# Kernel optimization log

Measured on AMD Instinct MI355X. Metric: run time of the kernel, lower is better.

## Reference

```python
import jax, jax.numpy as jnp
import numpy as np

D_MODEL = 1024
N_HEADS = 16
HEAD_DIM = D_MODEL // N_HEADS  # 64
BATCH = 2
SEQ = 2048
THETA = 10000.0


def _rope_tables(theta, d_k, max_seq_len):
    # matches RoPE.__init__: d = theta**(2*arange(d_k//2)/d_k); t = s / d
    inv = theta ** (2.0 * jnp.arange(0, d_k // 2, dtype=jnp.float32) / d_k)  # [d_k//2]
    s = jnp.arange(max_seq_len, dtype=jnp.float32)[:, None]  # [S,1]
    t = s / inv[None, :]  # [S, d_k//2]
    return jnp.sin(t), jnp.cos(t)


def setup_inputs() -> dict:
    key = jax.random.key(0)
    ks = jax.random.split(key, 5)
    std = np.sqrt(2.0 / (D_MODEL + D_MODEL))
    x = jax.random.normal(ks[0], (BATCH, SEQ, D_MODEL), dtype=jnp.float32)
    Wq = jax.random.normal(ks[1], (D_MODEL, D_MODEL), dtype=jnp.float32) * std
    Wk = jax.random.normal(ks[2], (D_MODEL, D_MODEL), dtype=jnp.float32) * std
    Wv = jax.random.normal(ks[3], (D_MODEL, D_MODEL), dtype=jnp.float32) * std
    Wo = jax.random.normal(ks[4], (D_MODEL, D_MODEL), dtype=jnp.float32) * std
    token_positions = jnp.arange(SEQ, dtype=jnp.int64)
    rope_sin, rope_cos = _rope_tables(THETA, HEAD_DIM, SEQ)
    return {"x": x, "token_positions": token_positions, "Wq": Wq, "Wk": Wk,
            "Wv": Wv, "Wo": Wo, "rope_sin": rope_sin, "rope_cos": rope_cos}


def _apply_rope(x, sin, cos):
    # x: [B, H, S, d_k]; sin/cos: [S, d_k//2] (gathered by token_positions)
    x1 = x[..., ::2]
    x2 = x[..., 1::2]
    x_even = x1 * cos - x2 * sin
    x_odd = x1 * sin + x2 * cos
    # interleave back: stack on last dim then flatten
    return jnp.stack([x_even, x_odd], axis=-1).reshape(x.shape)


def reference(x, token_positions, Wq, Wk, Wv, Wo, rope_sin, rope_cos):
    b, s, _ = x.shape
    h, d = N_HEADS, HEAD_DIM

    def proj(W):
        y = jnp.einsum('oi,bsi->bso', W, x)
        return y.reshape(b, s, h, d).transpose(0, 2, 1, 3)  # [b, h, s, d]

    q = proj(Wq)
    k = proj(Wk)
    v = proj(Wv)

    sin = rope_sin[token_positions]  # [s, d//2]
    cos = rope_cos[token_positions]
    q = _apply_rope(q, sin, cos)
    k = _apply_rope(k, sin, cos)

    # causal scaled-dot-product attention (FlashAttention.apply(..., True))
    scale = 1.0 / jnp.sqrt(jnp.asarray(d, dtype=x.dtype))
    scores = jnp.einsum('bhqd,bhkd->bhqk', q, k) * scale
    causal = jnp.tril(jnp.ones((s, s), dtype=bool))
    scores = jnp.where(causal, scores, jnp.finfo(x.dtype).min)
    attn = jax.nn.softmax(scores, axis=-1)
    out = jnp.einsum('bhqk,bhkd->bhqd', attn, v)  # [b, h, s, d]
    out = out.transpose(0, 2, 1, 3).reshape(b, s, h * d)
    return jnp.einsum('oi,bsi->bso', Wo, out)
```

## Files before the change

kernel.cpp:

```cpp
#include <hip/hip_runtime.h>
#include <hip/hip_bf16.h>
#include <math.h>

#define BATCH   2
#define S_LEN   2048
#define DM      1024
#define NH      16
#define HD      64
#define MROWS   4096

typedef __hip_bfloat16 bf16;
typedef __attribute__((ext_vector_type(8))) short short8;
typedef __attribute__((ext_vector_type(4))) float float4v;

#define QSCALE 0.18033688011112043f

#define WC_VM0   0x0F70
#define WC_VM4   0x0F74
#define WC_VM6   0x0F76
#define WC_VM8   0x0F78
#define WC_VM12  0x0F7C
#define WC_LGKM0 0xC07F

__device__ __forceinline__ short f2s(float x) {
    union { bf16 h; short s; } u; u.h = __float2bfloat16(x); return u.s;
}
__device__ __forceinline__ short8 load8(const void* p) {
    return *reinterpret_cast<const short8*>(p);
}
__device__ __forceinline__ void cvt8(const float* g, bf16* d) {
    float4v a = *reinterpret_cast<const float4v*>(g);
    float4v b = *reinterpret_cast<const float4v*>(g + 4);
    short8 r;
    r[0] = f2s(a[0]); r[1] = f2s(a[1]); r[2] = f2s(a[2]); r[3] = f2s(a[3]);
    r[4] = f2s(b[0]); r[5] = f2s(b[1]); r[6] = f2s(b[2]); r[7] = f2s(b[3]);
    *reinterpret_cast<short8*>(d) = r;
}
__device__ __forceinline__ void gll16(const void* g, void* l) {
    __builtin_amdgcn_global_load_lds(
        (const __attribute__((address_space(1))) unsigned int*)g,
        (__attribute__((address_space(3))) unsigned int*)l,
        16, 0, 0);
}
__device__ __forceinline__ unsigned pack2(float a, float b) {
    union { float f; unsigned u; } ua, ub;
    ua.f = a; ub.f = b;
    return ((ua.u + 0x8000u) >> 16) | ((ub.u + 0x8000u) & 0xFFFF0000u);
}

__global__ __launch_bounds__(256) void cvt_kernel(const float* __restrict__ x,
                                                  const float* __restrict__ wq,
                                                  const float* __restrict__ wk,
                                                  const float* __restrict__ wv,
                                                  const float* __restrict__ wo,
                                                  bf16* __restrict__ xb,
                                                  bf16* __restrict__ wqb,
                                                  bf16* __restrict__ wkb,
                                                  bf16* __restrict__ wvb,
                                                  bf16* __restrict__ wob) {
    const size_t i = ((size_t)blockIdx.x * 256 + threadIdx.x) * 8;
    const size_t NX = (size_t)MROWS * DM;
    const size_t NW = (size_t)DM * DM;
    if (i < NX)                { cvt8(x  + i,               xb  + i); }
    else if (i < NX + NW)      { cvt8(wq + (i - NX),        wqb + (i - NX)); }
    else if (i < NX + 2 * NW)  { cvt8(wk + (i - NX - NW),   wkb + (i - NX - NW)); }
    else if (i < NX + 3 * NW)  { cvt8(wv + (i - NX - 2*NW), wvb + (i - NX - 2*NW)); }
    else                       { cvt8(wo + (i - NX - 3*NW), wob + (i - NX - 3*NW)); }
}

__global__ __launch_bounds__(256) void qkv_gemm(const bf16* __restrict__ A,
                                                const bf16* __restrict__ Wqb,
                                                const bf16* __restrict__ Wkb,
                                                const bf16* __restrict__ Wvb,
                                                bf16* __restrict__ Qb, bf16* __restrict__ Kb,
                                                bf16* __restrict__ Vtb,
                                                const float* __restrict__ rsin,
                                                const float* __restrict__ rcos) {
    __shared__ short As[3][64 * 64];
    __shared__ short Bs[3][64 * 64];

    const int j    = threadIdx.x;
    const int w    = j >> 6;
    const int lane = j & 63;
    const int quad = lane >> 4;
    const int lid  = lane & 15;
    const int wm   = w & 1, wn = w >> 1;

    const int mb  = blockIdx.x * 128;
    const int sel = blockIdx.y >> 3;
    const int nb  = (blockIdx.y & 7) * 128;
    const bf16* W = (sel == 0) ? Wqb : (sel == 1) ? Wkb : Wvb;

    int sOff[2];
#pragma unroll
    for (int i = 0; i < 2; ++i) {
        const int u  = (i * 4 + w) * 64 + lane;
        const int rp = u >> 3;
        const int ch = (u & 7) ^ (rp & 7);
        const int gr = ((ch >> 2) << 6) + rp;
        const int gc = ch & 3;
        sOff[i] = gr * DM + gc * 8;
    }
    const bf16* baseA = A + (size_t)mb * DM;
    const bf16* baseB = W + (size_t)nb * DM;

#pragma unroll
    for (int t = 0; t < 2; ++t) {
#pragma unroll
        for (int i = 0; i < 2; ++i) gll16(baseA + t * 32 + sOff[i], &As[t][(i * 4 + w) * 512]);
#pragma unroll
        for (int i = 0; i < 2; ++i) gll16(baseB + t * 32 + sOff[i], &Bs[t][(i * 4 + w) * 512]);
    }

    int aRd[4], bRd[4];
#pragma unroll
    for (int t = 0; t < 4; ++t) {
        aRd[t] = (t * 16 + lid) * 64 + (((wm * 4 + quad) ^ (lid & 7)) * 8);
        bRd[t] = (t * 16 + lid) * 64 + (((wn * 4 + quad) ^ (lid & 7)) * 8);
    }

    float4v acc[4][4] = {};
    int buf = 0;
    for (int it = 0; it < 32; ++it) {
        __builtin_amdgcn_s_barrier();
        if (it < 30) {
            const int k0 = (it + 2) * 32;
            const int b = (buf + 2 >= 3) ? buf - 1 : buf + 2;
#pragma unroll
            for (int i = 0; i < 2; ++i) gll16(baseA + k0 + sOff[i], &As[b][(i * 4 + w) * 512]);
#pragma unroll
            for (int i = 0; i < 2; ++i) gll16(baseB + k0 + sOff[i], &Bs[b][(i * 4 + w) * 512]);
            __builtin_amdgcn_s_waitcnt(WC_VM8);
        } else if (it == 30) {
            __builtin_amdgcn_s_waitcnt(WC_VM4);
        } else {
            __builtin_amdgcn_s_waitcnt(WC_VM0);
        }
        __builtin_amdgcn_s_barrier();

        const short* as = As[buf];
        const short* bs = Bs[buf];
        short8 af[4], bfr[4];
#pragma unroll
        for (int mt = 0; mt < 4; ++mt) af[mt] = load8(&as[aRd[mt]]);
#pragma unroll
        for (int nt = 0; nt < 4; ++nt) bfr[nt] = load8(&bs[bRd[nt]]);
#pragma unroll
        for (int mt = 0; mt < 4; ++mt)
#pragma unroll
            for (int nt = 0; nt < 4; ++nt)
                acc[mt][nt] = __builtin_amdgcn_mfma_f32_16x16x32_bf16(af[mt], bfr[nt], acc[mt][nt], 0, 0, 0);
        buf = (buf == 2) ? 0 : buf + 1;
    }

#pragma unroll
    for (int mt = 0; mt < 4; ++mt) {
#pragma unroll
        for (int nt = 0; nt < 4; ++nt) {
            const int n = nb + wn * 64 + nt * 16 + lid;
            const int h = n >> 6, d = n & 63;
#pragma unroll
            for (int r = 0; r < 4; ++r) {
                const int m = mb + wm * 64 + mt * 16 + quad * 4 + r;
                const int s = m & (S_LEN - 1), bi = m >> 11;
                float val = acc[mt][nt][r];
                if (sel == 0) val *= QSCALE;
                float par = __shfl_xor(val, 1, 64);
                if (sel == 2) {
                    Vtb[(((size_t)bi * NH + h) * HD + d) * S_LEN + s] = __float2bfloat16(val);
                } else {
                    const float sn = rsin[s * 32 + (d >> 1)];
                    const float cs = rcos[s * 32 + (d >> 1)];
                    const float v = ((d & 1) == 0) ? val * cs - par * sn
                                                   : par * sn + val * cs;
                    bf16* dst = (sel == 0) ? Qb : Kb;
                    dst[(((size_t)bi * NH + h) * S_LEN + s) * HD + d] = __float2bfloat16(v);
                }
            }
        }
    }
}

__global__ __launch_bounds__(256) void out_gemm(const bf16* __restrict__ A,
                                                const bf16* __restrict__ W,
                                                float* __restrict__ out) {
    __shared__ short As[3][128 * 64];
    __shared__ short Bs[3][64 * 64];

    const int j    = threadIdx.x;
    const int w    = j >> 6;
    const int lane = j & 63;
    const int quad = lane >> 4;
    const int lid  = lane & 15;

    const int mb = blockIdx.x * 128;
    const int nb = blockIdx.y * 64;

    int aOff[4], bOff[2];
#pragma unroll
    for (int i = 0; i < 4; ++i) {
        const int u = i * 256 + j;
        const int r = u >> 3;
        const int c = (u & 7) ^ (r & 7);
        aOff[i] = r * DM + c * 8;
    }
#pragma unroll
    for (int i = 0; i < 2; ++i) {
        const int u = i * 256 + j;
        const int r = u >> 3;
        const int c = (u & 7) ^ (r & 7);
        bOff[i] = r * DM + c * 8;
    }
    const bf16* baseA = A + (size_t)mb * DM;
    const bf16* baseB = W + (size_t)nb * DM;

#pragma unroll
    for (int t = 0; t < 2; ++t) {
#pragma unroll
        for (int i = 0; i < 4; ++i) gll16(baseA + t * 64 + aOff[i], &As[t][(i * 256 + w * 64) * 8]);
#pragma unroll
        for (int i = 0; i < 2; ++i) gll16(baseB + t * 64 + bOff[i], &Bs[t][(i * 256 + w * 64) * 8]);
    }

    int aRd[2], bRd[4];
#pragma unroll
    for (int mt = 0; mt < 2; ++mt) {
        const int ra = w * 32 + mt * 16 + lid;
        aRd[mt] = ra * 64 + ((quad ^ (lid & 7)) * 8);
    }
#pragma unroll
    for (int nt = 0; nt < 4; ++nt) {
        const int rb = nt * 16 + lid;
        bRd[nt] = rb * 64 + ((quad ^ (lid & 7)) * 8);
    }

    float4v acc[2][4] = {};
    int buf = 0;
    for (int it = 0; it < 16; ++it) {
        __builtin_amdgcn_s_barrier();
        if (it < 14) {
            const int k0 = (it + 2) * 64;
            const int b = (buf + 2 >= 3) ? buf - 1 : buf + 2;
#pragma unroll
            for (int i = 0; i < 4; ++i) gll16(baseA + k0 + aOff[i], &As[b][(i * 256 + w * 64) * 8]);
#pragma unroll
            for (int i = 0; i < 2; ++i) gll16(baseB + k0 + bOff[i], &Bs[b][(i * 256 + w * 64) * 8]);
            __builtin_amdgcn_s_waitcnt(WC_VM12);
        } else if (it == 14) {
            __builtin_amdgcn_s_waitcnt(WC_VM6);
        } else {
            __builtin_amdgcn_s_waitcnt(WC_VM0);
        }
        __builtin_amdgcn_s_barrier();

        const short* as = As[buf];
        const short* bs = Bs[buf];
        short8 af[2][2], bfr[4][2];
#pragma unroll
        for (int mt = 0; mt < 2; ++mt)
#pragma unroll
            for (int ks = 0; ks < 2; ++ks) af[mt][ks] = load8(&as[aRd[mt] ^ (ks * 32)]);
#pragma unroll
        for (int nt = 0; nt < 4; ++nt)
#pragma unroll
            for (int ks = 0; ks < 2; ++ks) bfr[nt][ks] = load8(&bs[bRd[nt] ^ (ks * 32)]);
#pragma unroll
        for (int mt = 0; mt < 2; ++mt)
#pragma unroll
            for (int nt = 0; nt < 4; ++nt)
#pragma unroll
                for (int ks = 0; ks < 2; ++ks)
                    acc[mt][nt] = __builtin_amdgcn_mfma_f32_16x16x32_bf16(af[mt][ks], bfr[nt][ks], acc[mt][nt], 0, 0, 0);
        buf = (buf == 2) ? 0 : buf + 1;
    }

#pragma unroll
    for (int mt = 0; mt < 2; ++mt)
#pragma unroll
        for (int nt = 0; nt < 4; ++nt) {
            const int n = nb + nt * 16 + lid;
#pragma unroll
            for (int r = 0; r < 4; ++r) {
                const int m = mb + w * 32 + mt * 16 + quad * 4 + r;
                out[(size_t)m * DM + n] = acc[mt][nt][r];
            }
        }
}

__global__ __launch_bounds__(256) void flash6(const bf16* __restrict__ Q,
                                              const bf16* __restrict__ K,
                                              const bf16* __restrict__ Vt,
                                              bf16* __restrict__ att) {
    __shared__ short Ks[128 * 64];
    __shared__ short Vs[64 * 128];
    __shared__ short Pb[128 * 128];

    const int j    = threadIdx.x;
    const int w    = j >> 6;
    const int lane = j & 63;
    const int quad = lane >> 4;
    const int lid  = lane & 15;
    const int bh   = blockIdx.x;
    const int by   = blockIdx.y;
    const int qt   = (by < 8) ? (15 - by) : (by - 8);
    const int bi   = bh >> 4, h = bh & 15;
    const int qb   = qt * 128;

    const size_t bh_off = (size_t)bh * S_LEN * HD;
    const bf16* Qp = Q + bh_off;
    const bf16* Kp = K + bh_off;
    const bf16* Vp = Vt + bh_off;

    short8 aQ[2][2];
#pragma unroll
    for (int mm = 0; mm < 2; ++mm)
#pragma unroll
        for (int kf = 0; kf < 2; ++kf)
            aQ[mm][kf] = load8(Qp + (size_t)(qb + w * 32 + mm * 16 + lid) * HD + kf * 32 + quad * 8);

    int kOff[4], vOff[4];
#pragma unroll
    for (int i = 0; i < 4; ++i) {
        const int idx = (i * 4 + w) * 64 + lane;
        const int kr = idx >> 3, kc = (idx & 7) ^ (kr & 7);
        kOff[i] = kr * HD + kc * 8;
        const int vr = idx >> 4, vc = (idx & 15) ^ (vr & 15);
        vOff[i] = vr * S_LEN + vc * 8;
    }

    float4v accO[2][4] = {};
    float4v accS[2] = {};
    short8 ones;
#pragma unroll
    for (int t = 0; t < 8; ++t) ones[t] = (short)0x3F80;

    short8 kReg[4], vReg[4];
#pragma unroll
    for (int i = 0; i < 4; ++i) kReg[i] = load8(Kp + kOff[i]);
#pragma unroll
    for (int i = 0; i < 4; ++i) vReg[i] = load8(Vp + vOff[i]);

    const int nkt = qt + 1;
    for (int kti = 0; kti < nkt; ++kti) {
        __builtin_amdgcn_s_barrier();
#pragma unroll
        for (int i = 0; i < 4; ++i)
            *reinterpret_cast<short8*>(&Ks[(i * 4 + w) * 512 + lane * 8]) = kReg[i];
#pragma unroll
        for (int i = 0; i < 4; ++i)
            *reinterpret_cast<short8*>(&Vs[(i * 4 + w) * 512 + lane * 8]) = vReg[i];
        if (kti + 1 < nkt) {
            const int ktn = (kti + 1) * 128;
#pragma unroll
            for (int i = 0; i < 4; ++i) kReg[i] = load8(Kp + (size_t)ktn * HD + kOff[i]);
#pragma unroll
            for (int i = 0; i < 4; ++i) vReg[i] = load8(Vp + ktn + vOff[i]);
        }
        __builtin_amdgcn_s_waitcnt(WC_LGKM0);
        __builtin_amdgcn_s_barrier();

        const int kt = kti * 128;
        const bool diag = (kti == nkt - 1);

#pragma unroll
        for (int nt = 0; nt < 8; ++nt) {
            const int krow = nt * 16 + lid;
            short8 aK0 = load8(&Ks[krow * 64 + ((quad       ^ (lid & 7)) * 8)]);
            short8 aK1 = load8(&Ks[krow * 64 + (((4 + quad) ^ (lid & 7)) * 8)]);
#pragma unroll
            for (int mm = 0; mm < 2; ++mm) {
                float4v z = {};
                z = __builtin_amdgcn_mfma_f32_16x16x32_bf16(aK0, aQ[mm][0], z, 0, 0, 0);
                z = __builtin_amdgcn_mfma_f32_16x16x32_bf16(aK1, aQ[mm][1], z, 0, 0, 0);
                if (diag) {
                    const int qcol = qb + w * 32 + mm * 16 + lid;
#pragma unroll
                    for (int r = 0; r < 4; ++r)
                        if (kt + nt * 16 + quad * 4 + r > qcol) z[r] = -1e30f;
                }
                const float p0 = __builtin_amdgcn_exp2f(z[0]);
                const float p1 = __builtin_amdgcn_exp2f(z[1]);
                const float p2 = __builtin_amdgcn_exp2f(z[2]);
                const float p3 = __builtin_amdgcn_exp2f(z[3]);
                const int qrow = w * 32 + mm * 16 + lid;
                const int unit = (nt * 4 + quad) ^ ((lid & 7) * 2);
                uint2 pkd; pkd.x = pack2(p0, p1); pkd.y = pack2(p2, p3);
                *reinterpret_cast<uint2*>(&Pb[qrow * 128 + unit * 4]) = pkd;
            }
        }

        short8 aP[2][4];
#pragma unroll
        for (int mm = 0; mm < 2; ++mm) {
            const int qrow = w * 32 + mm * 16 + lid;
#pragma unroll
            for (int g = 0; g < 4; ++g) {
                const int u = (g * 8 + quad * 2) ^ ((lid & 7) * 2);
                aP[mm][g] = load8(&Pb[qrow * 128 + u * 4]);
                accS[mm] = __builtin_amdgcn_mfma_f32_16x16x32_bf16(aP[mm][g], ones, accS[mm], 0, 0, 0);
            }
        }
#pragma unroll
        for (int dt = 0; dt < 4; ++dt) {
#pragma unroll
            for (int g = 0; g < 4; ++g) {
                short8 bV = load8(&Vs[(dt * 16 + lid) * 128 + (((g * 4 + quad) ^ lid) * 8)]);
#pragma unroll
                for (int mm = 0; mm < 2; ++mm)
                    accO[mm][dt] = __builtin_amdgcn_mfma_f32_16x16x32_bf16(aP[mm][g], bV, accO[mm][dt], 0, 0, 0);
            }
        }
    }

#pragma unroll
    for (int mm = 0; mm < 2; ++mm) {
#pragma unroll
        for (int r = 0; r < 4; ++r) {
            const float inv = 1.0f / accS[mm][r];
            const int q = qb + w * 32 + mm * 16 + quad * 4 + r;
#pragma unroll
            for (int dt = 0; dt < 4; ++dt) {
                const int d = dt * 16 + lid;
                att[((size_t)bi * S_LEN + q) * DM + h * HD + d] =
                    __float2bfloat16(accO[mm][dt][r] * inv);
            }
        }
    }
}

extern "C" void kernel_launch(void* const* d_in, const int* in_sizes, int n_in,
                              void* d_out, int out_size, void* d_ws, size_t ws_size,
                              hipStream_t stream) {
    const float* x    = (const float*)d_in[0];
    const float* Wq   = (const float*)d_in[2];
    const float* Wk   = (const float*)d_in[3];
    const float* Wv   = (const float*)d_in[4];
    const float* Wo   = (const float*)d_in[5];
    const float* rsin = (const float*)d_in[6];
    const float* rcos = (const float*)d_in[7];
    float* out = (float*)d_out;

    char* ws = (char*)d_ws;
    const size_t MB = 1024 * 1024;
    bf16* Qb  = (bf16*)(ws + 0 * MB);
    bf16* Kb  = (bf16*)(ws + 8 * MB);
    bf16* Vtb = (bf16*)(ws + 16 * MB);
    bf16* xb  = (bf16*)(ws + 24 * MB);
    bf16* Wqb = (bf16*)(ws + 32 * MB);
    bf16* Wkb = (bf16*)(ws + 34 * MB);
    bf16* Wvb = (bf16*)(ws + 36 * MB);
    bf16* Wob = (bf16*)(ws + 38 * MB);
    bf16* atb = xb;

    cvt_kernel<<<4096, 256, 0, stream>>>(x, Wq, Wk, Wv, Wo, xb, Wqb, Wkb, Wvb, Wob);
    qkv_gemm<<<dim3(MROWS / 128, 24), 256, 0, stream>>>(xb, Wqb, Wkb, Wvb, Qb, Kb, Vtb, rsin, rcos);
    flash6<<<dim3(BATCH * NH, 16), 256, 0, stream>>>(Qb, Kb, Vtb, atb);
    out_gemm<<<dim3(MROWS / 128, DM / 64), 256, 0, stream>>>(atb, Wob, out);
}
```

Baseline: 181.9 us.

## Double-buffer K/V tiles in LDS and split P staging into two halves

K and V tiles now live in two LDS buffers. The next tile is written to the idle buffer after the current tile's compute, and global loads are issued two tiles ahead. This leaves one barrier per iteration instead of two and gives the global prefetch a full iteration to land. The softmax P staging buffer is halved by processing the 128 keys in two 64-key halves, which shrinks the aP register set and offsets some of the added K/V LDS. Total LDS per block grows, which could reduce how many blocks fit per CU.

```diff
diff --git a/kernel.cpp b/kernel.cpp
--- a/kernel.cpp
+++ b/kernel.cpp
@@ -291,9 +291,9 @@
                                               const bf16* __restrict__ K,
                                               const bf16* __restrict__ Vt,
                                               bf16* __restrict__ att) {
-    __shared__ short Ks[128 * 64];
-    __shared__ short Vs[64 * 128];
-    __shared__ short Pb[128 * 128];
+    __shared__ short Ks[2][128 * 64];
+    __shared__ short Vs[2][64 * 128];
+    __shared__ short Pb[128 * 64];
 
     const int j    = threadIdx.x;
     const int w    = j >> 6;
@@ -334,81 +334,105 @@
 #pragma unroll
     for (int t = 0; t < 8; ++t) ones[t] = (short)0x3F80;
 
+    const int nkt = qt + 1;
+
     short8 kReg[4], vReg[4];
 #pragma unroll
     for (int i = 0; i < 4; ++i) kReg[i] = load8(Kp + kOff[i]);
 #pragma unroll
     for (int i = 0; i < 4; ++i) vReg[i] = load8(Vp + vOff[i]);
-
-    const int nkt = qt + 1;
+#pragma unroll
+    for (int i = 0; i < 4; ++i)
+        *reinterpret_cast<short8*>(&Ks[0][(i * 4 + w) * 512 + lane * 8]) = kReg[i];
+#pragma unroll
+    for (int i = 0; i < 4; ++i)
+        *reinterpret_cast<short8*>(&Vs[0][(i * 4 + w) * 512 + lane * 8]) = vReg[i];
+    if (nkt > 1) {
+#pragma unroll
+        for (int i = 0; i < 4; ++i) kReg[i] = load8(Kp + (size_t)128 * HD + kOff[i]);
+#pragma unroll
+        for (int i = 0; i < 4; ++i) vReg[i] = load8(Vp + 128 + vOff[i]);
+    }
+    __builtin_amdgcn_s_waitcnt(WC_LGKM0);
+    __builtin_amdgcn_s_barrier();
+
     for (int kti = 0; kti < nkt; ++kti) {
-        __builtin_amdgcn_s_barrier();
-#pragma unroll
-        for (int i = 0; i < 4; ++i)
-            *reinterpret_cast<short8*>(&Ks[(i * 4 + w) * 512 + lane * 8]) = kReg[i];
-#pragma unroll
-        for (int i = 0; i < 4; ++i)
-            *reinterpret_cast<short8*>(&Vs[(i * 4 + w) * 512 + lane * 8]) = vReg[i];
-        if (kti + 1 < nkt) {
-            const int ktn = (kti + 1) * 128;
-#pragma unroll
-            for (int i = 0; i < 4; ++i) kReg[i] = load8(Kp + (size_t)ktn * HD + kOff[i]);
-#pragma unroll
-            for (int i = 0; i < 4; ++i) vReg[i] = load8(Vp + ktn + vOff[i]);
-        }
-        __builtin_amdgcn_s_waitcnt(WC_LGKM0);
-        __builtin_amdgcn_s_barrier();
-
+        const short* ks = Ks[kti & 1];
+        const short* vs = Vs[kti & 1];
         const int kt = kti * 128;
         const bool diag = (kti == nkt - 1);
 
 #pragma unroll
-        for (int nt = 0; nt < 8; ++nt) {
-            const int krow = nt * 16 + lid;
-            short8 aK0 = load8(&Ks[krow * 64 + ((quad       ^ (lid & 7)) * 8)]);
-            short8 aK1 = load8(&Ks[krow * 64 + (((4 + quad) ^ (lid & 7)) * 8)]);
+        for (int hf = 0; hf < 2; ++hf) {
+#pragma unroll
+            for (int nt2 = 0; nt2 < 4; ++nt2) {
+                const int nt = hf * 4 + nt2;
+                const int krow = nt * 16 + lid;
+                short8 aK0 = load8(&ks[krow * 64 + ((quad       ^ (lid & 7)) * 8)]);
+                short8 aK1 = load8(&ks[krow * 64 + (((4 + quad) ^ (lid & 7)) * 8)]);
+#pragma unroll
+                for (int mm = 0; mm < 2; ++mm) {
+                    float4v z = {};
+                    z = __builtin_amdgcn_mfma_f32_16x16x32_bf16(aK0, aQ[mm][0], z, 0, 0, 0);
+                    z = __builtin_amdgcn_mfma_f32_16x16x32_bf16(aK1, aQ[mm][1], z, 0, 0, 0);
+                    if (diag) {
+                        const int qcol = qb + w * 32 + mm * 16 + lid;
+#pragma unroll
+                        for (int r = 0; r < 4; ++r)
+                            if (kt + nt * 16 + quad * 4 + r > qcol) z[r] = -1e30f;
+                    }
+                    const float p0 = __builtin_amdgcn_exp2f(z[0]);
+                    const float p1 = __builtin_amdgcn_exp2f(z[1]);
+                    const float p2 = __builtin_amdgcn_exp2f(z[2]);
+                    const float p3 = __builtin_amdgcn_exp2f(z[3]);
+                    const int qrow = w * 32 + mm * 16 + lid;
+                    const int unit = (nt2 * 4 + quad) ^ ((lid & 7) * 2);
+                    uint2 pkd; pkd.x = pack2(p0, p1); pkd.y = pack2(p2, p3);
+                    *reinterpret_cast<uint2*>(&Pb[qrow * 64 + unit * 4]) = pkd;
+                }
+            }
+
+            short8 aP[2][2];
 #pragma unroll
             for (int mm = 0; mm < 2; ++mm) {
-                float4v z = {};
-                z = __builtin_amdgcn_mfma_f32_16x16x32_bf16(aK0, aQ[mm][0], z, 0, 0, 0);
-                z = __builtin_amdgcn_mfma_f32_16x16x32_bf16(aK1, aQ[mm][1], z, 0, 0, 0);
-                if (diag) {
-                    const int qcol = qb + w * 32 + mm * 16 + lid;
-#pragma unroll
-                    for (int r = 0; r < 4; ++r)
-                        if (kt + nt * 16 + quad * 4 + r > qcol) z[r] = -1e30f;
+                const int qrow = w * 32 + mm * 16 + lid;
+#pragma unroll
+                for (int g = 0; g < 2; ++g) {
+                    const int u = (g * 8 + quad * 2) ^ ((lid & 7) * 2);
+                    aP[mm][g] = load8(&Pb[qrow * 64 + u * 4]);
+                    accS[mm] = __builtin_amdgcn_mfma_f32_16x16x32_bf16(aP[mm][g], ones, accS[mm], 0, 0, 0);
                 }
-                const float p0 = __builtin_amdgcn_exp2f(z[0]);
-                const float p1 = __builtin_amdgcn_exp2f(z[1]);
-                const float p2 = __builtin_amdgcn_exp2f(z[2]);
-                const float p3 = __builtin_amdgcn_exp2f(z[3]);
-                const int qrow = w * 32 + mm * 16 + lid;
-                const int unit = (nt * 4 + quad) ^ ((lid & 7) * 2);
-                uint2 pkd; pkd.x = pack2(p0, p1); pkd.y = pack2(p2, p3);
-                *reinterpret_cast<uint2*>(&Pb[qrow * 128 + unit * 4]) = pkd;
-            }
-        }
-
-        short8 aP[2][4];
-#pragma unroll
-        for (int mm = 0; mm < 2; ++mm) {
-            const int qrow = w * 32 + mm * 16 + lid;
-#pragma unroll
-            for (int g = 0; g < 4; ++g) {
-                const int u = (g * 8 + quad * 2) ^ ((lid & 7) * 2);
-                aP[mm][g] = load8(&Pb[qrow * 128 + u * 4]);
-                accS[mm] = __builtin_amdgcn_mfma_f32_16x16x32_bf16(aP[mm][g], ones, accS[mm], 0, 0, 0);
-            }
-        }
-#pragma unroll
-        for (int dt = 0; dt < 4; ++dt) {
-#pragma unroll
-            for (int g = 0; g < 4; ++g) {
-                short8 bV = load8(&Vs[(dt * 16 + lid) * 128 + (((g * 4 + quad) ^ lid) * 8)]);
-#pragma unroll
-                for (int mm = 0; mm < 2; ++mm)
-                    accO[mm][dt] = __builtin_amdgcn_mfma_f32_16x16x32_bf16(aP[mm][g], bV, accO[mm][dt], 0, 0, 0);
-            }
+            }
+#pragma unroll
+            for (int dt = 0; dt < 4; ++dt) {
+#pragma unroll
+                for (int g = 0; g < 2; ++g) {
+                    const int gg = hf * 2 + g;
+                    short8 bV = load8(&vs[(dt * 16 + lid) * 128 + (((gg * 4 + quad) ^ lid) * 8)]);
+#pragma unroll
+                    for (int mm = 0; mm < 2; ++mm)
+                        accO[mm][dt] = __builtin_amdgcn_mfma_f32_16x16x32_bf16(aP[mm][g], bV, accO[mm][dt], 0, 0, 0);
+                }
+            }
+        }
+
+        if (kti + 1 < nkt) {
+            const int nb2 = (kti + 1) & 1;
+#pragma unroll
+            for (int i = 0; i < 4; ++i)
+                *reinterpret_cast<short8*>(&Ks[nb2][(i * 4 + w) * 512 + lane * 8]) = kReg[i];
+#pragma unroll
+            for (int i = 0; i < 4; ++i)
+                *reinterpret_cast<short8*>(&Vs[nb2][(i * 4 + w) * 512 + lane * 8]) = vReg[i];
+            if (kti + 2 < nkt) {
+                const int ktn = (kti + 2) * 128;
+#pragma unroll
+                for (int i = 0; i < 4; ++i) kReg[i] = load8(Kp + (size_t)ktn * HD + kOff[i]);
+#pragma unroll
+                for (int i = 0; i < 4; ++i) vReg[i] = load8(Vp + ktn + vOff[i]);
+            }
+            __builtin_amdgcn_s_waitcnt(WC_LGKM0);
+            __builtin_amdgcn_s_barrier();
         }
     }
 
```

Result: no change. 183.4 us (+0.8%).

## Switch QKV GEMM from triple-buffered K=32 to double-buffered K=64 tiles

Applied to the files above, without the earlier changes.

The QKV projection GEMM now stages 128x64 tiles of A and W per step instead of 128x32, using two LDS buffers instead of three. This halves the number of K iterations and their barrier pairs, and each step issues twice as many MFMAs. The swizzled LDS layout and read offsets are reworked to match. In exchange, prefetch depth drops from two stages to one and LDS use grows, so load latency is less hidden and occupancy may change.

```diff
diff --git a/kernel.cpp b/kernel.cpp
--- a/kernel.cpp
+++ b/kernel.cpp
@@ -76,8 +76,8 @@
                                                 bf16* __restrict__ Vtb,
                                                 const float* __restrict__ rsin,
                                                 const float* __restrict__ rcos) {
-    __shared__ short As[3][64 * 64];
-    __shared__ short Bs[3][64 * 64];
+    __shared__ short As[2][128 * 64];
+    __shared__ short Bs[2][128 * 64];
 
     const int j    = threadIdx.x;
     const int w    = j >> 6;
@@ -91,66 +91,64 @@
     const int nb  = (blockIdx.y & 7) * 128;
     const bf16* W = (sel == 0) ? Wqb : (sel == 1) ? Wkb : Wvb;
 
-    int sOff[2];
-#pragma unroll
-    for (int i = 0; i < 2; ++i) {
-        const int u  = (i * 4 + w) * 64 + lane;
-        const int rp = u >> 3;
-        const int ch = (u & 7) ^ (rp & 7);
-        const int gr = ((ch >> 2) << 6) + rp;
-        const int gc = ch & 3;
-        sOff[i] = gr * DM + gc * 8;
+    int sOff[4];
+#pragma unroll
+    for (int i = 0; i < 4; ++i) {
+        const int u = i * 256 + j;
+        const int r = u >> 3;
+        const int c = (u & 7) ^ (r & 7);
+        sOff[i] = r * DM + c * 8;
     }
     const bf16* baseA = A + (size_t)mb * DM;
     const bf16* baseB = W + (size_t)nb * DM;
 
 #pragma unroll
-    for (int t = 0; t < 2; ++t) {
-#pragma unroll
-        for (int i = 0; i < 2; ++i) gll16(baseA + t * 32 + sOff[i], &As[t][(i * 4 + w) * 512]);
-#pragma unroll
-        for (int i = 0; i < 2; ++i) gll16(baseB + t * 32 + sOff[i], &Bs[t][(i * 4 + w) * 512]);
-    }
+    for (int i = 0; i < 4; ++i) gll16(baseA + sOff[i], &As[0][(i * 256 + w * 64) * 8]);
+#pragma unroll
+    for (int i = 0; i < 4; ++i) gll16(baseB + sOff[i], &Bs[0][(i * 256 + w * 64) * 8]);
 
     int aRd[4], bRd[4];
 #pragma unroll
     for (int t = 0; t < 4; ++t) {
-        aRd[t] = (t * 16 + lid) * 64 + (((wm * 4 + quad) ^ (lid & 7)) * 8);
-        bRd[t] = (t * 16 + lid) * 64 + (((wn * 4 + quad) ^ (lid & 7)) * 8);
+        aRd[t] = (wm * 64 + t * 16 + lid) * 64 + ((quad ^ (lid & 7)) * 8);
+        bRd[t] = (wn * 64 + t * 16 + lid) * 64 + ((quad ^ (lid & 7)) * 8);
     }
 
     float4v acc[4][4] = {};
-    int buf = 0;
-    for (int it = 0; it < 32; ++it) {
-        __builtin_amdgcn_s_barrier();
-        if (it < 30) {
-            const int k0 = (it + 2) * 32;
-            const int b = (buf + 2 >= 3) ? buf - 1 : buf + 2;
-#pragma unroll
-            for (int i = 0; i < 2; ++i) gll16(baseA + k0 + sOff[i], &As[b][(i * 4 + w) * 512]);
-#pragma unroll
-            for (int i = 0; i < 2; ++i) gll16(baseB + k0 + sOff[i], &Bs[b][(i * 4 + w) * 512]);
+    for (int it = 0; it < 16; ++it) {
+        __builtin_amdgcn_s_barrier();
+        if (it < 15) {
+            const int k0 = (it + 1) * 64;
+            short* an = As[(it + 1) & 1];
+            short* bn = Bs[(it + 1) & 1];
+#pragma unroll
+            for (int i = 0; i < 4; ++i) gll16(baseA + k0 + sOff[i], &an[(i * 256 + w * 64) * 8]);
+#pragma unroll
+            for (int i = 0; i < 4; ++i) gll16(baseB + k0 + sOff[i], &bn[(i * 256 + w * 64) * 8]);
             __builtin_amdgcn_s_waitcnt(WC_VM8);
-        } else if (it == 30) {
-            __builtin_amdgcn_s_waitcnt(WC_VM4);
         } else {
             __builtin_amdgcn_s_waitcnt(WC_VM0);
         }
         __builtin_amdgcn_s_barrier();
 
-        const short* as = As[buf];
-        const short* bs = Bs[buf];
-        short8 af[4], bfr[4];
-#pragma unroll
-        for (int mt = 0; mt < 4; ++mt) af[mt] = load8(&as[aRd[mt]]);
-#pragma unroll
-        for (int nt = 0; nt < 4; ++nt) bfr[nt] = load8(&bs[bRd[nt]]);
+        const short* as = As[it & 1];
+        const short* bs = Bs[it & 1];
+        short8 af[4][2], bfr[4][2];
 #pragma unroll
         for (int mt = 0; mt < 4; ++mt)
 #pragma unroll
+            for (int ks = 0; ks < 2; ++ks) af[mt][ks] = load8(&as[aRd[mt] ^ (ks * 32)]);
+#pragma unroll
+        for (int nt = 0; nt < 4; ++nt)
+#pragma unroll
+            for (int ks = 0; ks < 2; ++ks) bfr[nt][ks] = load8(&bs[bRd[nt] ^ (ks * 32)]);
+#pragma unroll
+        for (int mt = 0; mt < 4; ++mt)
+#pragma unroll
             for (int nt = 0; nt < 4; ++nt)
-                acc[mt][nt] = __builtin_amdgcn_mfma_f32_16x16x32_bf16(af[mt], bfr[nt], acc[mt][nt], 0, 0, 0);
-        buf = (buf == 2) ? 0 : buf + 1;
+#pragma unroll
+                for (int ks = 0; ks < 2; ++ks)
+                    acc[mt][nt] = __builtin_amdgcn_mfma_f32_16x16x32_bf16(af[mt][ks], bfr[nt][ks], acc[mt][nt], 0, 0, 0);
     }
 
 #pragma unroll
```

New measurement: 197.7 us. +8.7%, slower.
